# Kernel tuning notes

Hardware: AMD Instinct MI355X
Metric: run time of the kernel (lower is better)

The kernel has to match this reference:

```python
import jax, jax.numpy as jnp
import numpy as np

B, C, D, H, W = 4, 128, 16, 16, 16
C8 = C // 8
TEXT = 256
N = D * H * W


def setup_inputs() -> dict:
    key = jax.random.key(0)
    ks = jax.random.split(key, 13)
    s = lambda fan: 1.0 / np.sqrt(fan)
    return {
        "x": jax.random.normal(ks[0], (B, C, D, H, W), jnp.float32),
        "text_emb": jax.random.normal(ks[1], (B, TEXT), jnp.float32),
        "Wq": jax.random.normal(ks[2], (C8, C), jnp.float32) * s(C),
        "bq": jax.random.normal(ks[3], (C8,), jnp.float32) * 0.01,
        "Wk": jax.random.normal(ks[4], (C8, C), jnp.float32) * s(C),
        "bk": jax.random.normal(ks[5], (C8,), jnp.float32) * 0.01,
        "Wv": jax.random.normal(ks[6], (C, C), jnp.float32) * s(C),
        "bv": jax.random.normal(ks[7], (C,), jnp.float32) * 0.01,
        "Wtk": jax.random.normal(ks[8], (C8, TEXT), jnp.float32) * s(TEXT),
        "btk": jax.random.normal(ks[9], (C8,), jnp.float32) * 0.01,
        "Wtv": jax.random.normal(ks[10], (C, TEXT), jnp.float32) * s(TEXT),
        "btv": jax.random.normal(ks[11], (C,), jnp.float32) * 0.01,
        # gamma is zero-init in the original; use a nonzero value so the
        # attention path contributes to the output (and to gradients).
        "gamma": jax.random.normal(ks[12], (1,), jnp.float32) * 0.1 + 0.5,
    }


def reference(x, text_emb, Wq, bq, Wk, bk, Wv, bv, Wtk, btk, Wtv, btv, gamma):
    b, c, d, h, w = x.shape
    n = d * h * w
    xf = x.reshape(b, c, n)                       # [B, C, N]
    # 1x1x1 convs == channel matmuls
    q = jnp.einsum('oc,bcn->bno', Wq, xf) + bq    # [B, N, C8]
    k = jnp.einsum('oc,bcn->bon', Wk, xf) + bk[None, :, None]  # [B, C8, N]
    v = jnp.einsum('oc,bcn->bon', Wv, xf) + bv[None, :, None]  # [B, C, N]
    # text-conditioned additive key/value (broadcast over all voxels)
    tk = (text_emb @ Wtk.T + btk)[:, :, None]     # [B, C8, 1]
    tv = (text_emb @ Wtv.T + btv)[:, :, None]     # [B, C, 1]
    k = k + tk
    v = v + tv
    # unscaled attention: softmax over keys
    scores = jnp.einsum('bno,bom->bnm', q, k)     # [B, N, N]
    attn = jax.nn.softmax(scores, axis=-1)
    # out[b,c,n] = sum_m v[b,c,m] * attn[b,n,m]
    out = jnp.einsum('bcm,bnm->bcn', v, attn).reshape(b, c, d, h, w)
    return gamma * out + x
```

## Files before the change

### kernel.cpp

```cpp
#include <hip/hip_runtime.h>
#include <math.h>

#define BB 4
#define CC 128
#define C8 16
#define TEXTN 256
#define NN 4096
#define WQB 32

typedef __attribute__((ext_vector_type(8))) __bf16 bf16x8;
typedef __attribute__((ext_vector_type(16))) float f32x16;

static __device__ __forceinline__ ushort f2bf(float f) {
  unsigned u = __builtin_bit_cast(unsigned, f);
  u += 0x7FFFu + ((u >> 16) & 1u);
  return (ushort)(u >> 16);
}

static __device__ __forceinline__ unsigned cvt_pk_bf16(float lo, float hi) {
  unsigned r;
  asm("v_cvt_pk_bf16_f32 %0, %1, %2" : "=v"(r) : "v"(lo), "v"(hi));
  return r;
}
static __device__ __forceinline__ void pl32swap(unsigned &a, unsigned &b) {
  asm("v_permlane32_swap_b32 %0, %1" : "+v"(a), "+v"(b));
}

__global__ __launch_bounds__(256) void k_text(
    const float* __restrict__ text, const float* __restrict__ Wtk,
    const float* __restrict__ btk, const float* __restrict__ Wtv,
    const float* __restrict__ btv, float* __restrict__ tkv) {
  __shared__ float ts[TEXTN];
  int b = blockIdx.x;
  for (int i = threadIdx.x; i < TEXTN; i += 256) ts[i] = text[b * TEXTN + i];
  __syncthreads();
  int o = threadIdx.x;
  if (o < 144) {
    const float* w;
    float acc;
    if (o < 16) { w = Wtk + o * TEXTN; acc = btk[o]; }
    else        { w = Wtv + (o - 16) * TEXTN; acc = btv[o - 16]; }
    #pragma unroll 8
    for (int t = 0; t < TEXTN; t++) acc += w[t] * ts[t];
    tkv[b * 144 + o] = acc;
  }
}

__global__ __launch_bounds__(320) void k_qkv(
    const float* __restrict__ x,
    const float* __restrict__ Wq, const float* __restrict__ bq,
    const float* __restrict__ Wk, const float* __restrict__ bk,
    const float* __restrict__ Wv, const float* __restrict__ bv,
    const float* __restrict__ tkv,
    ushort* __restrict__ qt, ushort* __restrict__ kt, ushort* __restrict__ vtB) {
  __shared__ __align__(16) ushort xs[64 * 128];
  int b = blockIdx.x >> 6;
  int n0 = (blockIdx.x & 63) * 64;
  int t = threadIdx.x;
  int w = t >> 6, lane = t & 63, l31 = lane & 31, hi = lane >> 5;

  for (int i = t; i < 2048; i += 320) {
    int c = i >> 4, n4 = i & 15;
    float4 xv = *(const float4*)&x[((size_t)b * CC + c) * NN + n0 + n4 * 4];
    float vals[4] = {xv.x, xv.y, xv.z, xv.w};
    #pragma unroll
    for (int k = 0; k < 4; ++k) {
      int n = n4 * 4 + k;
      xs[n * 128 + ((((c >> 3) ^ (n & 15)) << 3) | (c & 7))] = f2bf(vals[k]);
    }
  }

  const float* wrow;
  if (w == 0) wrow = (l31 < 16) ? (Wq + l31 * CC) : (Wk + (l31 - 16) * CC);
  else        wrow = Wv + (size_t)(32 * (w - 1) + l31) * CC;
  bf16x8 af[8];
  #pragma unroll
  for (int ks = 0; ks < 8; ++ks) {
    float4 u0 = *(const float4*)&wrow[ks * 16 + hi * 8];
    float4 u1 = *(const float4*)&wrow[ks * 16 + hi * 8 + 4];
    union { ushort u[8]; bf16x8 v; } tmp;
    tmp.u[0] = f2bf(u0.x); tmp.u[1] = f2bf(u0.y); tmp.u[2] = f2bf(u0.z); tmp.u[3] = f2bf(u0.w);
    tmp.u[4] = f2bf(u1.x); tmp.u[5] = f2bf(u1.y); tmp.u[6] = f2bf(u1.z); tmp.u[7] = f2bf(u1.w);
    af[ks] = tmp.v;
  }
  float badd[16];
  #pragma unroll
  for (int r = 0; r < 16; ++r) {
    int ol = (r & 3) + 8 * (r >> 2) + 4 * hi;
    if (w == 0) badd[r] = (ol < 16) ? bq[ol] : (bk[ol - 16] + tkv[b * 144 + ol - 16]);
    else { int c = 32 * (w - 1) + ol; badd[r] = bv[c] + tkv[b * 144 + 16 + c]; }
  }
  __syncthreads();

  #pragma unroll
  for (int n32 = 0; n32 < 2; ++n32) {
    int n = n32 * 32 + l31;
    int ng = n0 + n;
    bf16x8 bf[8];
    #pragma unroll
    for (int ks = 0; ks < 8; ++ks)
      bf[ks] = *(const bf16x8*)&xs[n * 128 + (((ks * 2 + hi) ^ (n & 15)) << 3)];
    f32x16 d;
    #pragma unroll
    for (int r = 0; r < 16; ++r) d[r] = 0.f;
    #pragma unroll
    for (int ks = 0; ks < 8; ++ks)
      d = __builtin_amdgcn_mfma_f32_32x32x16_bf16(af[ks], bf[ks], d, 0, 0, 0);
    #pragma unroll
    for (int g = 0; g < 4; ++g) {
      int o0 = 8 * g + 4 * hi;
      ushort4 pkv;
      pkv.x = f2bf(d[g * 4 + 0] + badd[g * 4 + 0]);
      pkv.y = f2bf(d[g * 4 + 1] + badd[g * 4 + 1]);
      pkv.z = f2bf(d[g * 4 + 2] + badd[g * 4 + 2]);
      pkv.w = f2bf(d[g * 4 + 3] + badd[g * 4 + 3]);
      if (w == 0) {
        if (o0 < 16) *(ushort4*)&qt[(b * NN + ng) * C8 + o0] = pkv;
        else         *(ushort4*)&kt[(b * NN + ng) * C8 + o0 - 16] = pkv;
      } else {
        int c0 = 32 * (w - 1) + o0;
        int base = b * (NN / 8) * CC * 8 + (ng >> 3) * (CC * 8) + (ng & 7);
        vtB[base + (c0 + 0) * 8] = pkv.x;
        vtB[base + (c0 + 1) * 8] = pkv.y;
        vtB[base + (c0 + 2) * 8] = pkv.z;
        vtB[base + (c0 + 3) * 8] = pkv.w;
      }
    }
  }
}

__global__ __launch_bounds__(256) void k_attn(
    const ushort* __restrict__ qt, const ushort* __restrict__ kt,
    const ushort* __restrict__ vtB, const float* __restrict__ x,
    const float* __restrict__ gamma_p, float* __restrict__ out) {
  __shared__ __align__(16) float mergeAcc[4][1024];
  __shared__ float mergeML[2][4][32];
  __shared__ float invGL[32];

  int b = blockIdx.x >> 7;
  int q0 = (blockIdx.x & 127) * WQB;
  int t = threadIdx.x;
  int w = t >> 6, lane = t & 63, l31 = lane & 31, hi = lane >> 5;

  const ushort* ktb = kt + (size_t)b * NN * C8;
  const ushort* vb  = vtB + (size_t)b * (NN / 8) * CC * 8;

  bf16x8 qf = *(const bf16x8*)&qt[((size_t)b * NN + q0 + l31) * C8 + hi * 8];

  f32x16 acc[4];
  #pragma unroll
  for (int cb = 0; cb < 4; ++cb)
    #pragma unroll
    for (int r = 0; r < 16; ++r) acc[cb][r] = 0.f;
  float m_run = -INFINITY, l_run = 0.f;

  bf16x8 kfA, kfB, vfA[8], vfB[8];

#define LDK(TT) (*(const bf16x8*)&ktb[(((TT) * 128 + w * 32 + l31)) * C8 + hi * 8])
#define LDV(TT, CB, KS) (*(const bf16x8*)&vb[(size_t)((TT) * 16 + w * 4 + (KS) * 2 + hi) * (CC * 8) + ((CB) * 32 + l31) * 8])

  kfA = LDK(0);
  #pragma unroll
  for (int cb = 0; cb < 4; ++cb) {
    vfA[cb * 2 + 0] = LDV(0, cb, 0);
    vfA[cb * 2 + 1] = LDV(0, cb, 1);
  }

#define STEP(CK, CV, NK, NV, TT)                                              \
  {                                                                           \
    int tn = ((TT) + 1) & 31;                                                 \
    NK = LDK(tn);                                                             \
    _Pragma("unroll")                                                         \
    for (int cb = 0; cb < 4; ++cb) {                                          \
      NV[cb * 2 + 0] = LDV(tn, cb, 0);                                        \
      NV[cb * 2 + 1] = LDV(tn, cb, 1);                                        \
    }                                                                         \
    f32x16 z;                                                                 \
    _Pragma("unroll")                                                         \
    for (int r = 0; r < 16; ++r) z[r] = 0.f;                                  \
    f32x16 s = __builtin_amdgcn_mfma_f32_32x32x16_bf16(CK, qf, z, 0, 0, 0);   \
    float mx = s[0];                                                          \
    _Pragma("unroll")                                                         \
    for (int r = 1; r < 16; ++r) mx = fmaxf(mx, s[r]);                        \
    mx = fmaxf(mx, __shfl_xor(mx, 32));                                       \
    bool resc = __any(mx > m_run + 8.f);                                      \
    float nm = m_run, corr = 1.f;                                             \
    if (resc) { nm = fmaxf(m_run, mx); corr = __expf(m_run - nm); }           \
    float p[16], ps = 0.f;                                                    \
    _Pragma("unroll")                                                         \
    for (int r = 0; r < 16; ++r) { p[r] = __expf(s[r] - nm); ps += p[r]; }    \
    ps += __shfl_xor(ps, 32);                                                 \
    if (resc) {                                                               \
      l_run *= corr;                                                          \
      _Pragma("unroll")                                                       \
      for (int cb = 0; cb < 4; ++cb)                                          \
        _Pragma("unroll")                                                     \
        for (int r = 0; r < 16; ++r) acc[cb][r] *= corr;                      \
      m_run = nm;                                                             \
    }                                                                         \
    l_run += ps;                                                              \
    bf16x8 pf0, pf1;                                                          \
    {                                                                         \
      unsigned a0 = cvt_pk_bf16(p[0], p[1]), b0 = cvt_pk_bf16(p[4], p[5]);    \
      unsigned c0 = cvt_pk_bf16(p[2], p[3]), d0 = cvt_pk_bf16(p[6], p[7]);    \
      pl32swap(a0, b0); pl32swap(c0, d0);                                     \
      union { unsigned u[4]; bf16x8 v; } u0; u0.u[0] = a0; u0.u[1] = c0;      \
      u0.u[2] = b0; u0.u[3] = d0; pf0 = u0.v;                                 \
      unsigned a1 = cvt_pk_bf16(p[8], p[9]), b1 = cvt_pk_bf16(p[12], p[13]);  \
      unsigned c1 = cvt_pk_bf16(p[10], p[11]), d1 = cvt_pk_bf16(p[14], p[15]);\
      pl32swap(a1, b1); pl32swap(c1, d1);                                     \
      union { unsigned u[4]; bf16x8 v; } u1; u1.u[0] = a1; u1.u[1] = c1;      \
      u1.u[2] = b1; u1.u[3] = d1; pf1 = u1.v;                                 \
    }                                                                         \
    _Pragma("unroll")                                                         \
    for (int cb = 0; cb < 4; ++cb) {                                          \
      acc[cb] = __builtin_amdgcn_mfma_f32_32x32x16_bf16(CV[cb * 2 + 0], pf0, acc[cb], 0, 0, 0); \
      acc[cb] = __builtin_amdgcn_mfma_f32_32x32x16_bf16(CV[cb * 2 + 1], pf1, acc[cb], 0, 0, 0); \
    }                                                                         \
  }

  for (int tt = 0; tt < 32; tt += 2) {
    STEP(kfA, vfA, kfB, vfB, tt)
    STEP(kfB, vfB, kfA, vfA, tt + 1)
  }
#undef STEP
#undef LDK
#undef LDV

  if (hi == 0) { mergeML[0][w][l31] = m_run; mergeML[1][w][l31] = l_run; }
  __syncthreads();
  float M = mergeML[0][0][l31];
  #pragma unroll
  for (int ww = 1; ww < 4; ++ww) M = fmaxf(M, mergeML[0][ww][l31]);
  float L = 0.f;
  #pragma unroll
  for (int ww = 0; ww < 4; ++ww)
    L += mergeML[1][ww][l31] * __expf(mergeML[0][ww][l31] - M);
  float scale = __expf(m_run - M);
  if (w == 0 && hi == 0) invGL[l31] = gamma_p[0] / L;

  int d0 = t * 4;
  int clocal = d0 >> 5, qq = d0 & 31;
  #pragma unroll
  for (int cb = 0; cb < 4; ++cb) {
    #pragma unroll
    for (int r = 0; r < 16; ++r)
      mergeAcc[w][((r & 3) + 8 * (r >> 2) + 4 * hi) * 32 + l31] = acc[cb][r] * scale;
    __syncthreads();
    float4 s0 = *(const float4*)&mergeAcc[0][d0];
    float4 s1 = *(const float4*)&mergeAcc[1][d0];
    float4 s2 = *(const float4*)&mergeAcc[2][d0];
    float4 s3 = *(const float4*)&mergeAcc[3][d0];
    float4 gl = *(const float4*)&invGL[qq];
    int c = cb * 32 + clocal;
    size_t base = ((size_t)b * CC + c) * NN + q0 + qq;
    float4 xv = *(const float4*)&x[base];
    float4 ov;
    ov.x = (s0.x + s1.x + s2.x + s3.x) * gl.x + xv.x;
    ov.y = (s0.y + s1.y + s2.y + s3.y) * gl.y + xv.y;
    ov.z = (s0.z + s1.z + s2.z + s3.z) * gl.z + xv.z;
    ov.w = (s0.w + s1.w + s2.w + s3.w) * gl.w + xv.w;
    *(float4*)&out[base] = ov;
    __syncthreads();
  }
}

extern "C" void kernel_launch(void* const* d_in, const int* in_sizes, int n_in,
                              void* d_out, int out_size, void* d_ws, size_t ws_size,
                              hipStream_t stream) {
  const float* x     = (const float*)d_in[0];
  const float* text  = (const float*)d_in[1];
  const float* Wq    = (const float*)d_in[2];
  const float* bq    = (const float*)d_in[3];
  const float* Wk    = (const float*)d_in[4];
  const float* bk    = (const float*)d_in[5];
  const float* Wv    = (const float*)d_in[6];
  const float* bv    = (const float*)d_in[7];
  const float* Wtk   = (const float*)d_in[8];
  const float* btk   = (const float*)d_in[9];
  const float* Wtv   = (const float*)d_in[10];
  const float* btv   = (const float*)d_in[11];
  const float* gamma = (const float*)d_in[12];
  float* outp = (float*)d_out;

  char* wsb = (char*)d_ws;
  float*  tkv = (float*)wsb;
  ushort* qt  = (ushort*)(wsb + 4096);
  ushort* kt  = (ushort*)(wsb + 4096 + 524288);
  ushort* vtB = (ushort*)(wsb + 4096 + 2 * 524288);

  k_text<<<BB, 256, 0, stream>>>(text, Wtk, btk, Wtv, btv, tkv);
  k_qkv<<<BB * NN / 64, 320, 0, stream>>>(x, Wq, bq, Wk, bk, Wv, bv, tkv, qt, kt, vtB);
  k_attn<<<BB * NN / WQB, 256, 0, stream>>>(qt, kt, vtB, x, gamma, outp);
}
```

Before: 57.25 us.

## Split attention keys across eight waves, use exp2 softmax, restructure x staging

Result: slower. 168.8 us (+194.9%).

```diff
diff --git a/kernel.cpp b/kernel.cpp
--- a/kernel.cpp
+++ b/kernel.cpp
@@ -7,14 +7,25 @@
 #define TEXTN 256
 #define NN 4096
 #define WQB 32
+#define NT 16
 
 typedef __attribute__((ext_vector_type(8))) __bf16 bf16x8;
 typedef __attribute__((ext_vector_type(16))) float f32x16;
+
+#define LOG2E 1.44269504088896340736f
 
 static __device__ __forceinline__ ushort f2bf(float f) {
   unsigned u = __builtin_bit_cast(unsigned, f);
   u += 0x7FFFu + ((u >> 16) & 1u);
   return (ushort)(u >> 16);
+}
+
+static __device__ __forceinline__ float exp2a(float x) {
+#if __has_builtin(__builtin_amdgcn_exp2f)
+  return __builtin_amdgcn_exp2f(x);
+#else
+  return exp2f(x);
+#endif
 }
 
 static __device__ __forceinline__ unsigned cvt_pk_bf16(float lo, float hi) {
@@ -59,15 +70,13 @@
   int t = threadIdx.x;
   int w = t >> 6, lane = t & 63, l31 = lane & 31, hi = lane >> 5;
 
-  for (int i = t; i < 2048; i += 320) {
-    int c = i >> 4, n4 = i & 15;
-    float4 xv = *(const float4*)&x[((size_t)b * CC + c) * NN + n0 + n4 * 4];
-    float vals[4] = {xv.x, xv.y, xv.z, xv.w};
-    #pragma unroll
-    for (int k = 0; k < 4; ++k) {
-      int n = n4 * 4 + k;
-      xs[n * 128 + ((((c >> 3) ^ (n & 15)) << 3) | (c & 7))] = f2bf(vals[k]);
-    }
+  for (int i = t; i < 1024; i += 320) {
+    int n = i & 63, ch = i >> 6;
+    union { ushort u[8]; uint4 v; } pk;
+    #pragma unroll
+    for (int j = 0; j < 8; ++j)
+      pk.u[j] = f2bf(x[((size_t)b * CC + ch * 8 + j) * NN + n0 + n]);
+    *(uint4*)&xs[n * 128 + ((ch ^ (n & 15)) << 3)] = pk.v;
   }
 
   const float* wrow;
@@ -109,11 +118,13 @@
     #pragma unroll
     for (int g = 0; g < 4; ++g) {
       int o0 = 8 * g + 4 * hi;
+      float v0 = d[g * 4 + 0] + badd[g * 4 + 0];
+      float v1 = d[g * 4 + 1] + badd[g * 4 + 1];
+      float v2 = d[g * 4 + 2] + badd[g * 4 + 2];
+      float v3 = d[g * 4 + 3] + badd[g * 4 + 3];
+      if (w == 0 && o0 < 16) { v0 *= LOG2E; v1 *= LOG2E; v2 *= LOG2E; v3 *= LOG2E; }
       ushort4 pkv;
-      pkv.x = f2bf(d[g * 4 + 0] + badd[g * 4 + 0]);
-      pkv.y = f2bf(d[g * 4 + 1] + badd[g * 4 + 1]);
-      pkv.z = f2bf(d[g * 4 + 2] + badd[g * 4 + 2]);
-      pkv.w = f2bf(d[g * 4 + 3] + badd[g * 4 + 3]);
+      pkv.x = f2bf(v0); pkv.y = f2bf(v1); pkv.z = f2bf(v2); pkv.w = f2bf(v3);
       if (w == 0) {
         if (o0 < 16) *(ushort4*)&qt[(b * NN + ng) * C8 + o0] = pkv;
         else         *(ushort4*)&kt[(b * NN + ng) * C8 + o0 - 16] = pkv;
@@ -129,12 +140,12 @@
   }
 }
 
-__global__ __launch_bounds__(256) void k_attn(
+__global__ __launch_bounds__(512, 4) void k_attn(
     const ushort* __restrict__ qt, const ushort* __restrict__ kt,
     const ushort* __restrict__ vtB, const float* __restrict__ x,
     const float* __restrict__ gamma_p, float* __restrict__ out) {
-  __shared__ __align__(16) float mergeAcc[4][1024];
-  __shared__ float mergeML[2][4][32];
+  __shared__ __align__(16) float mergeAcc[8][1024];
+  __shared__ float mergeML[2][8][32];
   __shared__ float invGL[32];
 
   int b = blockIdx.x >> 7;
@@ -156,8 +167,8 @@
 
   bf16x8 kfA, kfB, vfA[8], vfB[8];
 
-#define LDK(TT) (*(const bf16x8*)&ktb[(((TT) * 128 + w * 32 + l31)) * C8 + hi * 8])
-#define LDV(TT, CB, KS) (*(const bf16x8*)&vb[(size_t)((TT) * 16 + w * 4 + (KS) * 2 + hi) * (CC * 8) + ((CB) * 32 + l31) * 8])
+#define LDK(TT) (*(const bf16x8*)&ktb[((TT) * 256 + w * 32 + l31) * C8 + hi * 8])
+#define LDV(TT, CB, KS) (*(const bf16x8*)&vb[(size_t)((TT) * 32 + w * 4 + (KS) * 2 + hi) * (CC * 8) + ((CB) * 32 + l31) * 8])
 
   kfA = LDK(0);
   #pragma unroll
@@ -168,7 +179,7 @@
 
 #define STEP(CK, CV, NK, NV, TT)                                              \
   {                                                                           \
-    int tn = ((TT) + 1) & 31;                                                 \
+    int tn = ((TT) + 1) & (NT - 1);                                           \
     NK = LDK(tn);                                                             \
     _Pragma("unroll")                                                         \
     for (int cb = 0; cb < 4; ++cb) {                                          \
@@ -179,18 +190,18 @@
     _Pragma("unroll")                                                         \
     for (int r = 0; r < 16; ++r) z[r] = 0.f;                                  \
     f32x16 s = __builtin_amdgcn_mfma_f32_32x32x16_bf16(CK, qf, z, 0, 0, 0);   \
-    float mx = s[0];                                                          \
-    _Pragma("unroll")                                                         \
-    for (int r = 1; r < 16; ++r) mx = fmaxf(mx, s[r]);                        \
+    float x0 = fmaxf(s[0], s[1]),   x1 = fmaxf(s[2], s[3]);                   \
+    float x2 = fmaxf(s[4], s[5]),   x3 = fmaxf(s[6], s[7]);                   \
+    float x4 = fmaxf(s[8], s[9]),   x5 = fmaxf(s[10], s[11]);                 \
+    float x6 = fmaxf(s[12], s[13]), x7 = fmaxf(s[14], s[15]);                 \
+    x0 = fmaxf(x0, x1); x2 = fmaxf(x2, x3); x4 = fmaxf(x4, x5);               \
+    x6 = fmaxf(x6, x7);                                                       \
+    float mx = fmaxf(fmaxf(x0, x2), fmaxf(x4, x6));                           \
     mx = fmaxf(mx, __shfl_xor(mx, 32));                                       \
     bool resc = __any(mx > m_run + 8.f);                                      \
-    float nm = m_run, corr = 1.f;                                             \
-    if (resc) { nm = fmaxf(m_run, mx); corr = __expf(m_run - nm); }           \
-    float p[16], ps = 0.f;                                                    \
-    _Pragma("unroll")                                                         \
-    for (int r = 0; r < 16; ++r) { p[r] = __expf(s[r] - nm); ps += p[r]; }    \
-    ps += __shfl_xor(ps, 32);                                                 \
     if (resc) {                                                               \
+      float nm = fmaxf(m_run, mx);                                            \
+      float corr = exp2a(m_run - nm);                                         \
       l_run *= corr;                                                          \
       _Pragma("unroll")                                                       \
       for (int cb = 0; cb < 4; ++cb)                                          \
@@ -198,6 +209,16 @@
         for (int r = 0; r < 16; ++r) acc[cb][r] *= corr;                      \
       m_run = nm;                                                             \
     }                                                                         \
+    float p[16];                                                              \
+    _Pragma("unroll")                                                         \
+    for (int r = 0; r < 16; ++r) p[r] = exp2a(s[r] - m_run);                  \
+    float y0 = p[0] + p[1],   y1 = p[2] + p[3];                               \
+    float y2 = p[4] + p[5],   y3 = p[6] + p[7];                               \
+    float y4 = p[8] + p[9],   y5 = p[10] + p[11];                             \
+    float y6 = p[12] + p[13], y7 = p[14] + p[15];                             \
+    y0 += y1; y2 += y3; y4 += y5; y6 += y7;                                   \
+    float ps = (y0 + y2) + (y4 + y6);                                         \
+    ps += __shfl_xor(ps, 32);                                                 \
     l_run += ps;                                                              \
     bf16x8 pf0, pf1;                                                          \
     {                                                                         \
@@ -212,14 +233,16 @@
       union { unsigned u[4]; bf16x8 v; } u1; u1.u[0] = a1; u1.u[1] = c1;      \
       u1.u[2] = b1; u1.u[3] = d1; pf1 = u1.v;                                 \
     }                                                                         \
+    __builtin_amdgcn_s_setprio(1);                                            \
     _Pragma("unroll")                                                         \
     for (int cb = 0; cb < 4; ++cb) {                                          \
       acc[cb] = __builtin_amdgcn_mfma_f32_32x32x16_bf16(CV[cb * 2 + 0], pf0, acc[cb], 0, 0, 0); \
       acc[cb] = __builtin_amdgcn_mfma_f32_32x32x16_bf16(CV[cb * 2 + 1], pf1, acc[cb], 0, 0, 0); \
     }                                                                         \
-  }
-
-  for (int tt = 0; tt < 32; tt += 2) {
+    __builtin_amdgcn_s_setprio(0);                                            \
+  }
+
+  for (int tt = 0; tt < NT; tt += 2) {
     STEP(kfA, vfA, kfB, vfB, tt)
     STEP(kfB, vfB, kfA, vfA, tt + 1)
   }
@@ -231,15 +254,15 @@
   __syncthreads();
   float M = mergeML[0][0][l31];
   #pragma unroll
-  for (int ww = 1; ww < 4; ++ww) M = fmaxf(M, mergeML[0][ww][l31]);
+  for (int ww = 1; ww < 8; ++ww) M = fmaxf(M, mergeML[0][ww][l31]);
   float L = 0.f;
   #pragma unroll
-  for (int ww = 0; ww < 4; ++ww)
-    L += mergeML[1][ww][l31] * __expf(mergeML[0][ww][l31] - M);
-  float scale = __expf(m_run - M);
+  for (int ww = 0; ww < 8; ++ww)
+    L += mergeML[1][ww][l31] * exp2a(mergeML[0][ww][l31] - M);
+  float scale = exp2a(m_run - M);
   if (w == 0 && hi == 0) invGL[l31] = gamma_p[0] / L;
 
-  int d0 = t * 4;
+  int d0 = t * 2;
   int clocal = d0 >> 5, qq = d0 & 31;
   #pragma unroll
   for (int cb = 0; cb < 4; ++cb) {
@@ -247,20 +270,20 @@
     for (int r = 0; r < 16; ++r)
       mergeAcc[w][((r & 3) + 8 * (r >> 2) + 4 * hi) * 32 + l31] = acc[cb][r] * scale;
     __syncthreads();
-    float4 s0 = *(const float4*)&mergeAcc[0][d0];
-    float4 s1 = *(const float4*)&mergeAcc[1][d0];
-    float4 s2 = *(const float4*)&mergeAcc[2][d0];
-    float4 s3 = *(const float4*)&mergeAcc[3][d0];
-    float4 gl = *(const float4*)&invGL[qq];
+    float2 sum = *(const float2*)&mergeAcc[0][d0];
+    #pragma unroll
+    for (int ww = 1; ww < 8; ++ww) {
+      float2 sv = *(const float2*)&mergeAcc[ww][d0];
+      sum.x += sv.x; sum.y += sv.y;
+    }
+    float2 gl = *(const float2*)&invGL[qq];
     int c = cb * 32 + clocal;
     size_t base = ((size_t)b * CC + c) * NN + q0 + qq;
-    float4 xv = *(const float4*)&x[base];
-    float4 ov;
-    ov.x = (s0.x + s1.x + s2.x + s3.x) * gl.x + xv.x;
-    ov.y = (s0.y + s1.y + s2.y + s3.y) * gl.y + xv.y;
-    ov.z = (s0.z + s1.z + s2.z + s3.z) * gl.z + xv.z;
-    ov.w = (s0.w + s1.w + s2.w + s3.w) * gl.w + xv.w;
-    *(float4*)&out[base] = ov;
+    float2 xv = *(const float2*)&x[base];
+    float2 ov;
+    ov.x = sum.x * gl.x + xv.x;
+    ov.y = sum.y * gl.y + xv.y;
+    *(float2*)&out[base] = ov;
     __syncthreads();
   }
 }
@@ -291,5 +314,5 @@
 
   k_text<<<BB, 256, 0, stream>>>(text, Wtk, btk, Wtv, btv, tkv);
   k_qkv<<<BB * NN / 64, 320, 0, stream>>>(x, Wq, bq, Wk, bk, Wv, bv, tkv, qt, kt, vtB);
-  k_attn<<<BB * NN / WQB, 256, 0, stream>>>(qt, kt, vtB, x, gamma, outp);
-}
+  k_attn<<<BB * NN / WQB, 512, 0, stream>>>(qt, kt, vtB, x, gamma, outp);
+}
```
